# Optimization experiments

Hardware: AMD Instinct MI355X
Metric: run time of the kernel (lower is better)

## Reference

```python
import jax, jax.numpy as jnp
import numpy as np

C = 256
CQK = C // 8


def setup_inputs() -> dict:
    key = jax.random.key(0)
    ks = jax.random.split(key, 8)
    B, H, W = 4, 64, 64
    inputs = jax.random.normal(ks[0], (B, H, W, C), dtype=jnp.float32)
    s = 1.0 / np.sqrt(C)
    Wq = jax.random.normal(ks[1], (C, CQK), dtype=jnp.float32) * s
    bq = jnp.zeros((CQK,), dtype=jnp.float32)
    Wk = jax.random.normal(ks[2], (C, CQK), dtype=jnp.float32) * s
    bk = jnp.zeros((CQK,), dtype=jnp.float32)
    Wv = jax.random.normal(ks[3], (C, C), dtype=jnp.float32) * s
    bv = jnp.zeros((C,), dtype=jnp.float32)
    gamma = jnp.float32(0.7)  # nonzero so attention branch contributes
    return {"inputs": inputs, "Wq": Wq, "bq": bq, "Wk": Wk, "bk": bk,
            "Wv": Wv, "bv": bv, "gamma": gamma}


def reference(inputs, Wq, bq, Wk, bk, Wv, bv, gamma):
    B, H, W, Cin = inputs.shape
    N = H * W
    x = inputs.reshape(B, N, Cin)
    # 1x1 convs == per-pixel channel matmuls
    q = x @ Wq + bq                      # (B, N, C//8)
    k = x @ Wk + bk                      # (B, N, C//8)
    v = x @ Wv + bv                      # (B, N, C)
    energy = jnp.einsum('bnd,bmd->bnm', q, k)   # (B, N, N), no scale (faithful)
    attn = jax.nn.softmax(energy, axis=-1)
    x_out = jnp.einsum('bnm,bmc->bnc', attn, v)  # (B, N, C)
    out = gamma * x_out.reshape(B, H, W, Cin) + inputs
    return out
```

## Files before the change

### kernel.cpp

```cpp
#include <hip/hip_runtime.h>
#include <hip/hip_bf16.h>

#define B_ 4
#define N_ 4096
#define C_ 256
#define D_ 32
#define LOG2E 1.44269504088896340736f
#define MFMA16 __builtin_amdgcn_mfma_f32_16x16x32_bf16

typedef __attribute__((ext_vector_type(8))) short short8;
typedef __attribute__((ext_vector_type(4))) short short4v;
typedef __attribute__((ext_vector_type(4))) float float4v;

__device__ inline short f2bf_rne(float f) {
  unsigned u = __builtin_bit_cast(unsigned, f);
  u += 0x7FFFu + ((u >> 16) & 1u);
  return (short)(u >> 16);
}
__device__ inline float bf2f(short s) {
  unsigned u = ((unsigned)(unsigned short)s) << 16;
  return __builtin_bit_cast(float, u);
}
__device__ inline float fast_exp2(float x) { return __builtin_amdgcn_exp2f(x); }

__device__ inline short4v pk4_bf16(float p0, float p1, float p2, float p3) {
  union { unsigned u[2]; short4v s; } r;
  asm("v_cvt_pk_bf16_f32 %0, %1, %2" : "=v"(r.u[0]) : "v"(p0), "v"(p1));
  asm("v_cvt_pk_bf16_f32 %0, %1, %2" : "=v"(r.u[1]) : "v"(p2), "v"(p3));
  return r.s;
}

__global__ __launch_bounds__(256) void cast_w_kernel(
    const float* __restrict__ Wq, const float* __restrict__ Wk,
    const float* __restrict__ Wv, short* __restrict__ WtF) {
  int i  = blockIdx.x * 256 + threadIdx.x;
  int j  = i & 7;
  int l  = (i >> 3) & 63;
  int ks = (i >> 9) & 7;
  int nb = i >> 12;
  int n  = nb * 16 + (l & 15);
  int k  = ks * 32 + ((l >> 4) << 3) + j;
  float v;
  if (n < 32)      v = Wq[k * 32 + n] * LOG2E;
  else if (n < 64) v = Wk[k * 32 + (n - 32)];
  else             v = Wv[k * 256 + (n - 64)];
  WtF[i] = f2bf_rne(v);
}

__global__ __launch_bounds__(256, 2) void proj_kernel(
    const float* __restrict__ x, const short* __restrict__ WtF,
    const float* __restrict__ bq, const float* __restrict__ bk,
    const float* __restrict__ bv,
    short* __restrict__ qb, short* __restrict__ kF, short* __restrict__ vF) {
  int blk = blockIdx.x;
  int b  = blk >> 7;
  int r0 = (blk & 127) * 32;
  int t  = threadIdx.x;
  int w  = t >> 6;
  int l  = t & 63;
  int lc = l & 15;
  int q4 = l >> 4;

  __shared__ __align__(16) short sA[32][272];
  __shared__ __align__(16) short sV[256][40];
  __shared__ __align__(16) short sK[32][36];

  {
    const float* xb = x + (size_t)(b * N_ + r0) * C_;
#pragma unroll
    for (int ch = 0; ch < 8; ch++) {
      int f   = ch * 256 + t;
      int row = f >> 6;
      int col = (f & 63) * 4;
      float4v v = *(const float4v*)(xb + f * 4);
      short4v s = pk4_bf16(v[0], v[1], v[2], v[3]);
      *(short4v*)(&sA[row][col]) = s;
    }
  }
  __syncthreads();

  float4v acc[10];
#pragma unroll
  for (int i = 0; i < 10; i++) { acc[i][0] = 0.f; acc[i][1] = 0.f; acc[i][2] = 0.f; acc[i][3] = 0.f; }

  const short* wbase = WtF + w * 4096 + l * 8;

#define LOADW(B0, B1, B2, B3, B4, KS)                       \
  B0 = *(const short8*)(wbase + (KS) * 512 + 0 * 16384);    \
  B1 = *(const short8*)(wbase + (KS) * 512 + 1 * 16384);    \
  B2 = *(const short8*)(wbase + (KS) * 512 + 2 * 16384);    \
  B3 = *(const short8*)(wbase + (KS) * 512 + 3 * 16384);    \
  B4 = *(const short8*)(wbase + (KS) * 512 + 4 * 16384);

#define DO_MFMA(A0, A1, B0, B1, B2, B3, B4)                 \
  acc[0] = MFMA16(A0, B0, acc[0], 0, 0, 0);                 \
  acc[1] = MFMA16(A1, B0, acc[1], 0, 0, 0);                 \
  acc[2] = MFMA16(A0, B1, acc[2], 0, 0, 0);                 \
  acc[3] = MFMA16(A1, B1, acc[3], 0, 0, 0);                 \
  acc[4] = MFMA16(A0, B2, acc[4], 0, 0, 0);                 \
  acc[5] = MFMA16(A1, B2, acc[5], 0, 0, 0);                 \
  acc[6] = MFMA16(A0, B3, acc[6], 0, 0, 0);                 \
  acc[7] = MFMA16(A1, B3, acc[7], 0, 0, 0);                 \
  acc[8] = MFMA16(A0, B4, acc[8], 0, 0, 0);                 \
  acc[9] = MFMA16(A1, B4, acc[9], 0, 0, 0);

  short8 wA0, wA1, wA2, wA3, wA4, wB0, wB1, wB2, wB3, wB4;
  LOADW(wA0, wA1, wA2, wA3, wA4, 0)
#pragma unroll
  for (int kk = 0; kk < 8; kk += 2) {
    short8 a00 = *(const short8*)(&sA[lc][kk * 32 + q4 * 8]);
    short8 a01 = *(const short8*)(&sA[16 + lc][kk * 32 + q4 * 8]);
    LOADW(wB0, wB1, wB2, wB3, wB4, kk + 1)
    DO_MFMA(a00, a01, wA0, wA1, wA2, wA3, wA4)
    short8 a10 = *(const short8*)(&sA[lc][(kk + 1) * 32 + q4 * 8]);
    short8 a11 = *(const short8*)(&sA[16 + lc][(kk + 1) * 32 + q4 * 8]);
    LOADW(wA0, wA1, wA2, wA3, wA4, kk + 2)
    DO_MFMA(a10, a11, wB0, wB1, wB2, wB3, wB4)
  }
#undef LOADW
#undef DO_MFMA

  {
    float bias0 = (w < 2) ? bq[w * 16 + lc] * LOG2E : bk[(w - 2) * 16 + lc];
#pragma unroll
    for (int rt = 0; rt < 2; rt++) {
      if (w < 2) {
#pragma unroll
        for (int r = 0; r < 4; r++) {
          int row = rt * 16 + q4 * 4 + r;
          qb[(size_t)(b * N_ + r0 + row) * D_ + w * 16 + lc] =
              f2bf_rne(acc[rt][r] + bias0);
        }
      } else {
#pragma unroll
        for (int r = 0; r < 4; r++) {
          int row = rt * 16 + q4 * 4 + r;
          sK[row][(w - 2) * 16 + lc] = f2bf_rne(acc[rt][r] + bias0);
        }
      }
    }
#pragma unroll
    for (int nbo = 1; nbo < 5; nbo++) {
      float bias = bv[(nbo - 1) * 64 + w * 16 + lc];
#pragma unroll
      for (int rt = 0; rt < 2; rt++) {
        float4v a = acc[nbo * 2 + rt];
        short4v pk = pk4_bf16(a[0] + bias, a[1] + bias, a[2] + bias, a[3] + bias);
        *(short4v*)(&sV[(nbo - 1) * 64 + w * 16 + lc][rt * 16 + q4 * 4]) = pk;
      }
    }
  }
  __syncthreads();

  int kt  = r0 >> 6;
  int ks0 = (r0 >> 5) & 1;

  {
    size_t tb2 = ((size_t)(b * 64 + kt) * 32 + ks0 * 16) * 512;
    int cb = t >> 4;
#pragma unroll
    for (int k = 0; k < 4; k++) {
      int p = (t & 15) * 4 + k;
      int j = p >> 4, i = p & 15;
      short8 vv = *(const short8*)(&sV[cb * 16 + i][j * 8]);
      *(short8*)(vF + tb2 + (size_t)t * 32 + k * 8) = vv;
    }
  }
  if (t < 128) {
    int fr = t >> 6, ll = t & 63;
    int kv = fr * 16 + (ll & 15), dg = ll >> 4;
    size_t tbk = ((size_t)(b * 64 + kt) * 4 + ks0 * 2) * 512;
    short8 kv8 = *(const short8*)(&sK[kv][dg * 8]);
    *(short8*)(kF + tbk + (size_t)t * 8) = kv8;
  }
}

__global__ __launch_bounds__(512, 4) void flash_partial_kernel(
    const short* __restrict__ qb, const short* __restrict__ kF,
    const short* __restrict__ vF, short* __restrict__ obuf,
    float* __restrict__ lbuf) {
  int blk = blockIdx.x;
  int b  = blk & 3;
  int hb = (blk >> 2) & 1;
  int qt = blk >> 3;
  int r0 = qt * 64;
  int t  = threadIdx.x;
  int w  = t >> 6;
  int l  = t & 63;
  int lc = l & 15;
  int q4 = l >> 4;
  int rq = w & 3;
  bool qkw = (w < 4);

  __shared__ __align__(16) short sPn[2][4096];

  int p = (b * 64 + qt) * 2 + hb;

  short8 qf = *(const short8*)(qb + (size_t)(b * N_ + r0 + rq * 16 + lc) * D_ + q4 * 8);

  const short* kbp = kF + ((size_t)(b * 64 + hb * 32) * 4) * 512 + l * 8;
  const short* vbp = vF + ((size_t)(b * 64 + hb * 32) * 32 + 2 * w) * 512 + l * 8;

  short8 kC0, kC1, kC2, kC3;
  short8 vX00, vX01, vX10, vX11;
  short8 vY00, vY01, vY10, vY11;

  kC0 = *(const short8*)(kbp + 0);
  kC1 = *(const short8*)(kbp + 512);
  kC2 = *(const short8*)(kbp + 1024);
  kC3 = *(const short8*)(kbp + 1536);
  vX00 = *(const short8*)(vbp + 0);
  vX01 = *(const short8*)(vbp + 512);
  vX10 = *(const short8*)(vbp + 8192);
  vX11 = *(const short8*)(vbp + 8704);

  float4v O[8];
#pragma unroll
  for (int i = 0; i < 8; i++) { O[i][0] = 0.f; O[i][1] = 0.f; O[i][2] = 0.f; O[i][3] = 0.f; }
  float l_part = 0.f;

  if (qkw) __builtin_amdgcn_s_setprio(1);

  int qkbase = (rq * 2) * 512 + (((q4 >> 1) * 16) + lc) * 8 + (q4 & 1) * 4;

#define K_RELOAD(TI)                                                           \
  { size_t o_ = (size_t)(TI) * 2048;                                           \
    kC0 = *(const short8*)(kbp + o_);                                          \
    kC1 = *(const short8*)(kbp + o_ + 512);                                    \
    kC2 = *(const short8*)(kbp + o_ + 1024);                                   \
    kC3 = *(const short8*)(kbp + o_ + 1536); }

#define QK_STEP(SPB, VALID)                                                    \
  { float4v z; z[0] = 0.f; z[1] = 0.f; z[2] = 0.f; z[3] = 0.f;                 \
    float4v S0 = MFMA16(kC0, qf, z, 0, 0, 0);                                  \
    float4v S1 = MFMA16(kC1, qf, z, 0, 0, 0);                                  \
    float4v S2 = MFMA16(kC2, qf, z, 0, 0, 0);                                  \
    float4v S3 = MFMA16(kC3, qf, z, 0, 0, 0);                                  \
    short* rowp = &sPn[SPB][qkbase];                                           \
    float ts = 0.f;                                                            \
    { float p0 = fast_exp2(S0[0]), p1 = fast_exp2(S0[1]);                      \
      float p2 = fast_exp2(S0[2]), p3 = fast_exp2(S0[3]);                      \
      ts += (p0 + p1) + (p2 + p3);                                             \
      *(short4v*)(rowp + 0) = pk4_bf16(p0, p1, p2, p3); }                      \
    { float p0 = fast_exp2(S1[0]), p1 = fast_exp2(S1[1]);                      \
      float p2 = fast_exp2(S1[2]), p3 = fast_exp2(S1[3]);                      \
      ts += (p0 + p1) + (p2 + p3);                                             \
      *(short4v*)(rowp + 256) = pk4_bf16(p0, p1, p2, p3); }                    \
    { float p0 = fast_exp2(S2[0]), p1 = fast_exp2(S2[1]);                      \
      float p2 = fast_exp2(S2[2]), p3 = fast_exp2(S2[3]);                      \
      ts += (p0 + p1) + (p2 + p3);                                             \
      *(short4v*)(rowp + 512) = pk4_bf16(p0, p1, p2, p3); }                    \
    { float p0 = fast_exp2(S3[0]), p1 = fast_exp2(S3[1]);                      \
      float p2 = fast_exp2(S3[2]), p3 = fast_exp2(S3[3]);                      \
      ts += (p0 + p1) + (p2 + p3);                                             \
      *(short4v*)(rowp + 768) = pk4_bf16(p0, p1, p2, p3); }                    \
    if (VALID) l_part += ts; }

#define PV_STEP(SPB, V00, V01, V10, V11)                                       \
  { _Pragma("unroll")                                                          \
    for (int rt = 0; rt < 4; rt++) {                                           \
      short8 pf0 = *(const short8*)(&sPn[SPB][(rt * 2 + 0) * 512 + l * 8]);    \
      short8 pf1 = *(const short8*)(&sPn[SPB][(rt * 2 + 1) * 512 + l * 8]);    \
      O[rt * 2 + 0] = MFMA16(pf0, V00, O[rt * 2 + 0], 0, 0, 0);                \
      O[rt * 2 + 0] = MFMA16(pf1, V10, O[rt * 2 + 0], 0, 0, 0);                \
      O[rt * 2 + 1] = MFMA16(pf0, V01, O[rt * 2 + 1], 0, 0, 0);                \
      O[rt * 2 + 1] = MFMA16(pf1, V11, O[rt * 2 + 1], 0, 0, 0);                \
    } }

  if (qkw) {
    QK_STEP(0, true)
    K_RELOAD(1)
  }
  __syncthreads();

  for (int ti = 0; ti < 32; ti += 2) {
    int n1 = ti + 1;
    int n2 = (ti + 2 < 32) ? ti + 2 : 31;
    bool v2 = (ti + 2 < 32);
    int n3 = (ti + 3 < 32) ? ti + 3 : 31;

    { size_t vo = (size_t)n1 * 16384;
      vY00 = *(const short8*)(vbp + vo);
      vY01 = *(const short8*)(vbp + vo + 512);
      vY10 = *(const short8*)(vbp + vo + 8192);
      vY11 = *(const short8*)(vbp + vo + 8704); }
    if (qkw) {
      QK_STEP(1, true)
      K_RELOAD(n2)
    }
    PV_STEP(0, vX00, vX01, vX10, vX11)
    __syncthreads();

    { size_t vo = (size_t)n2 * 16384;
      vX00 = *(const short8*)(vbp + vo);
      vX01 = *(const short8*)(vbp + vo + 512);
      vX10 = *(const short8*)(vbp + vo + 8192);
      vX11 = *(const short8*)(vbp + vo + 8704); }
    if (qkw) {
      QK_STEP(0, v2)
      K_RELOAD(n3)
    }
    PV_STEP(1, vY00, vY01, vY10, vY11)
    __syncthreads();
  }
#undef K_RELOAD
#undef QK_STEP
#undef PV_STEP

  {
    short* ob = obuf + ((size_t)p * 64 + w * 8) * 256 + l * 4;
#pragma unroll
    for (int a = 0; a < 8; a++) {
      float4v o = O[a];
      *(short4v*)(ob + a * 256) = pk4_bf16(o[0], o[1], o[2], o[3]);
    }
  }
  if (qkw) {
    float l_tot = l_part + __shfl_xor(l_part, 16, 64);
    l_tot += __shfl_xor(l_tot, 32, 64);
    if (q4 == 0) lbuf[(size_t)p * 64 + rq * 16 + lc] = l_tot;
  }
}

__global__ __launch_bounds__(256) void merge_kernel(
    const short* __restrict__ obuf, const float* __restrict__ lbuf,
    const float* __restrict__ xin, const float* __restrict__ gptr,
    float* __restrict__ out) {
  int blk2 = blockIdx.x;
  int blk  = blk2 >> 1;
  int h    = blk2 & 1;
  int t    = threadIdx.x;
  float g  = *gptr;

  __shared__ float sS[32][260];
  __shared__ float sGLinv[32];

  const short* o0 = obuf + (size_t)(blk * 2 + 0) * 16384;
  const short* o1 = obuf + (size_t)(blk * 2 + 1) * 16384;
  const float* l0 = lbuf + (size_t)(blk * 2 + 0) * 64;
  const float* l1 = lbuf + (size_t)(blk * 2 + 1) * 64;
  size_t gbase = (size_t)blk * 16384;

  if (t < 32)
    sGLinv[t] = g * __builtin_amdgcn_rcpf(l0[32 * h + t] + l1[32 * h + t]);

#pragma unroll
  for (int j = 0; j < 4; j++) {
    int gdx    = j * 256 + t;
    int chunk  = gdx >> 7;
    int within = gdx & 127;
    int offs   = (chunk * 8 + 4 * h) * 256 + within * 8;
    short8 a8 = *(const short8*)(o0 + offs);
    short8 c8 = *(const short8*)(o1 + offs);
    int s_in  = within >> 5;
    int pos8  = within & 31;
    int rt    = 2 * h + (s_in >> 1);
    int cbo   = s_in & 1;
    int chB   = chunk * 32 + cbo * 16;
#pragma unroll
    for (int e = 0; e < 8; e++) {
      int lane = pos8 * 2 + (e >> 2);
      int r    = e & 3;
      int row  = (rt & 1) * 16 + (lane >> 4) * 4 + r;
      int ch   = chB + (lane & 15);
      sS[row][ch] = bf2f(a8[e]) + bf2f(c8[e]);
    }
  }
  __syncthreads();

#pragma unroll
  for (int j = 0; j < 8; j++) {
    int gdx = j * 1024 + t * 4;
    int row = gdx >> 8;
    int ch  = gdx & 255;
    float gl = sGLinv[row];
    size_t gi = gbase + (size_t)(32 * h) * 256 + gdx;
    float4v xv = *(const float4v*)(xin + gi);
    float4v sv = *(const float4v*)(&sS[row][ch]);
    float4v ov;
#pragma unroll
    for (int e = 0; e < 4; e++) ov[e] = sv[e] * gl + xv[e];
    *(float4v*)(out + gi) = ov;
  }
}

extern "C" void kernel_launch(void* const* d_in, const int* in_sizes, int n_in,
                              void* d_out, int out_size, void* d_ws, size_t ws_size,
                              hipStream_t stream) {
  const float* x     = (const float*)d_in[0];
  const float* Wq    = (const float*)d_in[1];
  const float* bq    = (const float*)d_in[2];
  const float* Wk    = (const float*)d_in[3];
  const float* bk    = (const float*)d_in[4];
  const float* Wv    = (const float*)d_in[5];
  const float* bv    = (const float*)d_in[6];
  const float* gamma = (const float*)d_in[7];
  float* out = (float*)d_out;

  char* ws = (char*)d_ws;
  short* qb   = (short*)ws;
  short* kF   = (short*)(ws + (1u << 20));
  short* vF   = (short*)(ws + (2u << 20));
  short* WtF  = (short*)(ws + (10u << 20));
  short* obuf = (short*)(ws + (11u << 20));
  float* lbuf = (float*)(ws + (28u << 20));

  hipLaunchKernelGGL(cast_w_kernel,        dim3(320), dim3(256), 0, stream, Wq, Wk, Wv, WtF);
  hipLaunchKernelGGL(proj_kernel,          dim3(512), dim3(256), 0, stream, x, WtF, bq, bk, bv, qb, kF, vF);
  hipLaunchKernelGGL(flash_partial_kernel, dim3(512), dim3(512), 0, stream, qb, kF, vF, obuf, lbuf);
  hipLaunchKernelGGL(merge_kernel,         dim3(512), dim3(256), 0, stream, obuf, lbuf, x, gamma, out);
}
```

Before: 139.8 us.

## Split QK^T/exp work across all eight waves instead of four

Before, only waves 0-3 computed the QK^T scores and exponentials for each 64-key tile while all eight waves did the PV accumulation. Now every wave computes half of the key tile: two MFMAs and eight exp2 per step instead of four and sixteen. The row sums are combined across the two halves through shared memory at the end. This is meant to balance the per-wave load and shorten the critical path before each barrier, at the cost of an extra synchronisation and small LDS array, with priority raised only around the QK section.

```diff
diff --git a/kernel.cpp b/kernel.cpp
--- a/kernel.cpp
+++ b/kernel.cpp
@@ -190,25 +190,24 @@
   int lc = l & 15;
   int q4 = l >> 4;
   int rq = w & 3;
-  bool qkw = (w < 4);
+  int kh = w >> 2;
 
   __shared__ __align__(16) short sPn[2][4096];
+  __shared__ float sL[4][16];
 
   int p = (b * 64 + qt) * 2 + hb;
 
   short8 qf = *(const short8*)(qb + (size_t)(b * N_ + r0 + rq * 16 + lc) * D_ + q4 * 8);
 
-  const short* kbp = kF + ((size_t)(b * 64 + hb * 32) * 4) * 512 + l * 8;
+  const short* kbp = kF + ((size_t)(b * 64 + hb * 32) * 4) * 512 + kh * 1024 + l * 8;
   const short* vbp = vF + ((size_t)(b * 64 + hb * 32) * 32 + 2 * w) * 512 + l * 8;
 
-  short8 kC0, kC1, kC2, kC3;
+  short8 kC0, kC1;
   short8 vX00, vX01, vX10, vX11;
   short8 vY00, vY01, vY10, vY11;
 
   kC0 = *(const short8*)(kbp + 0);
   kC1 = *(const short8*)(kbp + 512);
-  kC2 = *(const short8*)(kbp + 1024);
-  kC3 = *(const short8*)(kbp + 1536);
   vX00 = *(const short8*)(vbp + 0);
   vX01 = *(const short8*)(vbp + 512);
   vX10 = *(const short8*)(vbp + 8192);
@@ -219,24 +218,19 @@
   for (int i = 0; i < 8; i++) { O[i][0] = 0.f; O[i][1] = 0.f; O[i][2] = 0.f; O[i][3] = 0.f; }
   float l_part = 0.f;
 
-  if (qkw) __builtin_amdgcn_s_setprio(1);
-
   int qkbase = (rq * 2) * 512 + (((q4 >> 1) * 16) + lc) * 8 + (q4 & 1) * 4;
 
 #define K_RELOAD(TI)                                                           \
   { size_t o_ = (size_t)(TI) * 2048;                                           \
     kC0 = *(const short8*)(kbp + o_);                                          \
-    kC1 = *(const short8*)(kbp + o_ + 512);                                    \
-    kC2 = *(const short8*)(kbp + o_ + 1024);                                   \
-    kC3 = *(const short8*)(kbp + o_ + 1536); }
+    kC1 = *(const short8*)(kbp + o_ + 512); }
 
 #define QK_STEP(SPB, VALID)                                                    \
-  { float4v z; z[0] = 0.f; z[1] = 0.f; z[2] = 0.f; z[3] = 0.f;                 \
+  { __builtin_amdgcn_s_setprio(1);                                             \
+    float4v z; z[0] = 0.f; z[1] = 0.f; z[2] = 0.f; z[3] = 0.f;                 \
     float4v S0 = MFMA16(kC0, qf, z, 0, 0, 0);                                  \
     float4v S1 = MFMA16(kC1, qf, z, 0, 0, 0);                                  \
-    float4v S2 = MFMA16(kC2, qf, z, 0, 0, 0);                                  \
-    float4v S3 = MFMA16(kC3, qf, z, 0, 0, 0);                                  \
-    short* rowp = &sPn[SPB][qkbase];                                           \
+    short* rowp = &sPn[SPB][qkbase + kh * 512];                                \
     float ts = 0.f;                                                            \
     { float p0 = fast_exp2(S0[0]), p1 = fast_exp2(S0[1]);                      \
       float p2 = fast_exp2(S0[2]), p3 = fast_exp2(S0[3]);                      \
@@ -246,14 +240,7 @@
       float p2 = fast_exp2(S1[2]), p3 = fast_exp2(S1[3]);                      \
       ts += (p0 + p1) + (p2 + p3);                                             \
       *(short4v*)(rowp + 256) = pk4_bf16(p0, p1, p2, p3); }                    \
-    { float p0 = fast_exp2(S2[0]), p1 = fast_exp2(S2[1]);                      \
-      float p2 = fast_exp2(S2[2]), p3 = fast_exp2(S2[3]);                      \
-      ts += (p0 + p1) + (p2 + p3);                                             \
-      *(short4v*)(rowp + 512) = pk4_bf16(p0, p1, p2, p3); }                    \
-    { float p0 = fast_exp2(S3[0]), p1 = fast_exp2(S3[1]);                      \
-      float p2 = fast_exp2(S3[2]), p3 = fast_exp2(S3[3]);                      \
-      ts += (p0 + p1) + (p2 + p3);                                             \
-      *(short4v*)(rowp + 768) = pk4_bf16(p0, p1, p2, p3); }                    \
+    __builtin_amdgcn_s_setprio(0);                                             \
     if (VALID) l_part += ts; }
 
 #define PV_STEP(SPB, V00, V01, V10, V11)                                       \
@@ -267,10 +254,8 @@
       O[rt * 2 + 1] = MFMA16(pf1, V11, O[rt * 2 + 1], 0, 0, 0);                \
     } }
 
-  if (qkw) {
-    QK_STEP(0, true)
-    K_RELOAD(1)
-  }
+  QK_STEP(0, true)
+  K_RELOAD(1)
   __syncthreads();
 
   for (int ti = 0; ti < 32; ti += 2) {
@@ -284,10 +269,8 @@
       vY01 = *(const short8*)(vbp + vo + 512);
       vY10 = *(const short8*)(vbp + vo + 8192);
       vY11 = *(const short8*)(vbp + vo + 8704); }
-    if (qkw) {
-      QK_STEP(1, true)
-      K_RELOAD(n2)
-    }
+    QK_STEP(1, true)
+    K_RELOAD(n2)
     PV_STEP(0, vX00, vX01, vX10, vX11)
     __syncthreads();
 
@@ -296,10 +279,8 @@
       vX01 = *(const short8*)(vbp + vo + 512);
       vX10 = *(const short8*)(vbp + vo + 8192);
       vX11 = *(const short8*)(vbp + vo + 8704); }
-    if (qkw) {
-      QK_STEP(0, v2)
-      K_RELOAD(n3)
-    }
+    QK_STEP(0, v2)
+    K_RELOAD(n3)
     PV_STEP(1, vY00, vY01, vY10, vY11)
     __syncthreads();
   }
@@ -315,10 +296,13 @@
       *(short4v*)(ob + a * 256) = pk4_bf16(o[0], o[1], o[2], o[3]);
     }
   }
-  if (qkw) {
+  {
     float l_tot = l_part + __shfl_xor(l_part, 16, 64);
     l_tot += __shfl_xor(l_tot, 32, 64);
-    if (q4 == 0) lbuf[(size_t)p * 64 + rq * 16 + lc] = l_tot;
+    if (kh == 0 && q4 == 0) sL[rq][lc] = l_tot;
+    __syncthreads();
+    if (kh == 1 && q4 == 0)
+      lbuf[(size_t)p * 64 + rq * 16 + lc] = l_tot + sL[rq][lc];
   }
 }
 
```

Result: no change. 140.2 us (+0.3%).
